# Kernel tuning notes

Hardware: AMD Instinct MI355X
Metric: run time of the kernel (lower is better)

The kernel has to match this reference:

```python
import jax, jax.numpy as jnp
import numpy as np

D_IN, D_HID, D_OUT = 256, 512, 256
N_EXPERTS, TOP_K = 64, 2
B, S = 8, 4096


def setup_inputs() -> dict:
    key = jax.random.key(0)
    ks = jax.random.split(key, 8)
    scale_in = 1.0 / np.sqrt(D_IN)
    scale_hid = 1.0 / np.sqrt(D_HID)
    return {
        "x": jax.random.normal(ks[0], (B, S, D_IN), dtype=jnp.float32),
        "Wr": jax.random.uniform(ks[1], (D_IN, N_EXPERTS), jnp.float32, -scale_in, scale_in),
        "br": jax.random.uniform(ks[2], (N_EXPERTS,), jnp.float32, -scale_in, scale_in),
        "W1": jax.random.uniform(ks[3], (N_EXPERTS, D_IN, D_HID), jnp.float32, -scale_in, scale_in),
        "b1": jax.random.uniform(ks[4], (N_EXPERTS, D_HID), jnp.float32, -scale_in, scale_in),
        "W2": jax.random.uniform(ks[5], (N_EXPERTS, D_HID, D_OUT), jnp.float32, -scale_hid, scale_hid),
        "b2": jax.random.uniform(ks[6], (N_EXPERTS, D_OUT), jnp.float32, -scale_hid, scale_hid),
    }


def reference(x, Wr, br, W1, b1, W2, b2):
    Bx, Sx, D = x.shape
    xf = x.reshape(-1, D)                                  # [T, D]
    T = xf.shape[0]
    E = Wr.shape[1]
    logits = xf @ Wr + br                                  # [T, E]
    topk_logits, topk_idx = jax.lax.top_k(logits, TOP_K)   # [T, K]
    gates = jax.nn.softmax(topk_logits, axis=1)            # softmax over selected k
    # dense combine weights: zero except at selected experts
    combine = jnp.zeros((T, E), xf.dtype).at[
        jnp.arange(T)[:, None], topk_idx].add(gates)       # [T, E]
    out = jnp.zeros((T, W2.shape[-1]), xf.dtype)
    for e in range(E):  # fixed small expert loop; each token weighted by combine mask
        h = jax.nn.relu(xf @ W1[e] + b1[e])                # [T, D_HID]
        y = h @ W2[e] + b2[e]                              # [T, D_OUT]
        out = out + combine[:, e:e + 1] * y
    return out.reshape(Bx, Sx, -1)
```

## Files before the change

### kernel.cpp

```cpp
#include <hip/hip_runtime.h>
#include <stdint.h>

#define T_TOK 32768
#define DIN   256
#define DHID  512
#define DOUT  256
#define NEXP  64
#define L1_SLOTS 8
#define L2_SLOTS 8
#define ROUTER_BLOCKS (T_TOK / 64)
#define PREP_BLOCKS   8192
#define OUTZ_BLOCKS   512
#define XBF_BLOCKS    1024
#define L1_BLOCKS (NEXP * 4 * L1_SLOTS)
#define L2_BLOCKS (NEXP * 2 * L2_SLOTS)

typedef __attribute__((ext_vector_type(8))) short short8;
typedef __attribute__((ext_vector_type(4))) float f32x4;

#define OFF_W1F   0u
#define OFF_W2F   16777216u
#define OFF_BASE  33554432u
#define OFF_CNT   (OFF_BASE + 0u)
#define OFF_CUR   (OFF_BASE + 256u)
#define OFF_OFFS  (OFF_BASE + 512u)
#define OFF_TOPKE (OFF_BASE + 2048u)
#define OFF_TOPKG (OFF_TOPKE + 262144u)
#define OFF_PERM  (OFF_TOPKG + 262144u)
#define OFF_PGATE (OFF_PERM + 262144u)
#define OFF_XBF   (OFF_BASE + 2097152u)
#define OFF_H     (OFF_XBF + 16777216u)

__device__ __forceinline__ unsigned short f2bf(float f) {
    union { float f; unsigned u; } a; a.f = f;
    unsigned u = a.u;
    u += 0x7fffu + ((u >> 16) & 1u);
    return (unsigned short)(u >> 16);
}
__device__ __forceinline__ unsigned pack2(float a, float b) {
    return (unsigned)f2bf(a) | ((unsigned)f2bf(b) << 16);
}

__device__ __forceinline__ void async_copy16(const uint4* g, uint4* l) {
    __builtin_amdgcn_global_load_lds(
        (const __attribute__((address_space(1))) unsigned int*)g,
        (__attribute__((address_space(3))) unsigned int*)l, 16, 0, 0);
}

__global__ __launch_bounds__(256) void router_prep(const float* __restrict__ x,
                                                   const float* __restrict__ Wr,
                                                   const float* __restrict__ br,
                                                   const float* __restrict__ W1,
                                                   const float* __restrict__ W2,
                                                   uint4* __restrict__ W1f,
                                                   uint4* __restrict__ W2f,
                                                   int* __restrict__ topk_e,
                                                   float* __restrict__ topk_g,
                                                   int* __restrict__ cnt,
                                                   float4* __restrict__ outz,
                                                   unsigned* __restrict__ xbf) {
    __shared__ float xl[64][68];
    __shared__ float wt[64][68];
    __shared__ int lcnt[NEXP];
    int tid = threadIdx.x;

    if (blockIdx.x >= ROUTER_BLOCKS + PREP_BLOCKS + OUTZ_BLOCKS) {
        int blk = blockIdx.x - (ROUTER_BLOCKS + PREP_BLOCKS + OUTZ_BLOCKS);
        const float2* xs = (const float2*)x;
#pragma unroll
        for (int k = 0; k < 16; ++k) {
            int o = blk * 4096 + k * 256 + tid;
            float2 v = xs[o];
            xbf[o] = pack2(v.x, v.y);
        }
        return;
    }
    if (blockIdx.x >= ROUTER_BLOCKS + PREP_BLOCKS) {
        int base = (blockIdx.x - (ROUTER_BLOCKS + PREP_BLOCKS)) * 256 + tid;
        float4 z = {0.0f, 0.0f, 0.0f, 0.0f};
#pragma unroll
        for (int i = 0; i < 16; ++i) outz[base + i * (OUTZ_BLOCKS * 256)] = z;
        return;
    }
    if (blockIdx.x >= ROUTER_BLOCKS) {
        int g = (blockIdx.x - ROUTER_BLOCKS) * 256 + tid;
        int isW2 = g >> 20;
        int gg = g & ((1 << 20) - 1);
        int l = gg & 63;
        int t = gg >> 6;
        int e = t >> 8;
        int rem = t & 255;
        int quad = l >> 4, lr = l & 15;
        float v[8];
        if (!isW2) {
            int nt = rem >> 3, kt = rem & 7;
            int kb = kt * 32 + quad * 8;
            int n = nt * 16 + lr;
            const float* s = W1 + (size_t)e * DIN * DHID + n;
#pragma unroll
            for (int j = 0; j < 8; ++j) v[j] = s[(size_t)(kb + j) * DHID];
        } else {
            int nt = rem >> 4, kt = rem & 15;
            int kb = kt * 32 + quad * 8;
            int n = nt * 16 + lr;
            const float* s = W2 + (size_t)e * DHID * DOUT + n;
#pragma unroll
            for (int j = 0; j < 8; ++j) v[j] = s[(size_t)(kb + j) * DOUT];
        }
        uint4 o;
        o.x = pack2(v[0], v[1]); o.y = pack2(v[2], v[3]);
        o.z = pack2(v[4], v[5]); o.w = pack2(v[6], v[7]);
        (isW2 ? W2f : W1f)[gg] = o;
        return;
    }

    if (tid < NEXP) lcnt[tid] = 0;
    int a = tid >> 4;
    int bcol = tid & 15;
    int tok0 = blockIdx.x * 64;
    float c[4][4];
#pragma unroll
    for (int i = 0; i < 4; ++i)
#pragma unroll
        for (int j = 0; j < 4; ++j) c[i][j] = 0.0f;

    for (int chunk = 0; chunk < 4; ++chunk) {
        int d0 = chunk * 64;
        {
            int tok = tid >> 2, off = (tid & 3) * 16;
            const float4* s = (const float4*)(x + (size_t)(tok0 + tok) * DIN + d0 + off);
            float4* d = (float4*)&xl[tok][off];
#pragma unroll
            for (int i = 0; i < 4; ++i) d[i] = s[i];
        }
        {
            int dd = tid >> 2, ecol = (tid & 3) * 16;
            const float* s = Wr + (size_t)(d0 + dd) * NEXP + ecol;
#pragma unroll
            for (int j = 0; j < 16; ++j) wt[ecol + j][dd] = s[j];
        }
        __syncthreads();
#pragma unroll 4
        for (int d = 0; d < 64; d += 4) {
            float4 xv[4], wv[4];
#pragma unroll
            for (int i = 0; i < 4; ++i) xv[i] = *(const float4*)&xl[bcol + i * 16][d];
#pragma unroll
            for (int j = 0; j < 4; ++j) wv[j] = *(const float4*)&wt[a + j * 16][d];
#pragma unroll
            for (int i = 0; i < 4; ++i)
#pragma unroll
                for (int j = 0; j < 4; ++j) {
                    c[i][j] = fmaf(xv[i].x, wv[j].x, c[i][j]);
                    c[i][j] = fmaf(xv[i].y, wv[j].y, c[i][j]);
                    c[i][j] = fmaf(xv[i].z, wv[j].z, c[i][j]);
                    c[i][j] = fmaf(xv[i].w, wv[j].w, c[i][j]);
                }
        }
        __syncthreads();
    }
#pragma unroll
    for (int i = 0; i < 4; ++i)
#pragma unroll
        for (int j = 0; j < 4; ++j)
            xl[bcol + i * 16][a + j * 16] = c[i][j] + br[a + j * 16];
    __syncthreads();

    int w = tid >> 6, lane = tid & 63;
    for (int ti = 0; ti < 16; ++ti) {
        int tl = w * 16 + ti;
        float acc = xl[tl][lane];
        float v = acc; int idx = lane;
#pragma unroll
        for (int m = 32; m; m >>= 1) {
            float ov = __shfl_xor(v, m); int oi = __shfl_xor(idx, m);
            if (ov > v || (ov == v && oi < idx)) { v = ov; idx = oi; }
        }
        int e0 = idx; float l0 = v;
        float v2 = (lane == e0) ? -3.4e38f : acc; int idx2 = lane;
#pragma unroll
        for (int m = 32; m; m >>= 1) {
            float ov = __shfl_xor(v2, m); int oi = __shfl_xor(idx2, m);
            if (ov > v2 || (ov == v2 && oi < idx2)) { v2 = ov; idx2 = oi; }
        }
        if (lane == 0) {
            int t = tok0 + tl;
            float ex = expf(v2 - l0);
            float g1 = ex / (1.0f + ex);
            topk_e[2 * t] = e0; topk_e[2 * t + 1] = idx2;
            topk_g[2 * t] = 1.0f - g1; topk_g[2 * t + 1] = g1;
            atomicAdd(&lcnt[e0], 1);
            atomicAdd(&lcnt[idx2], 1);
        }
    }
    __syncthreads();
    if (tid < NEXP) atomicAdd(&cnt[tid], lcnt[tid]);
}

__global__ __launch_bounds__(256) void scatter_kernel(const int* __restrict__ topk_e,
                                                      const float* __restrict__ topk_g,
                                                      const int* __restrict__ cnt,
                                                      int* __restrict__ cursor,
                                                      int* __restrict__ perm,
                                                      float* __restrict__ pgate,
                                                      int* __restrict__ offs_g) {
    __shared__ int lcnt[NEXP], lbase[NEXP], sOffs[NEXP];
    int tid = threadIdx.x;
    if (tid < NEXP) lcnt[tid] = 0;
    if (tid < 64) {
        int c = cnt[tid];
        int ic = c;
#pragma unroll
        for (int d = 1; d < 64; d <<= 1) {
            int vc = __shfl_up(ic, d);
            if (tid >= d) ic += vc;
        }
        sOffs[tid] = ic - c;
        if (blockIdx.x == 0) {
            offs_g[tid] = ic - c;
            if (tid == 63) offs_g[64] = ic;
        }
    }
    __syncthreads();
    int t = blockIdx.x * 256 + tid;
    int e0 = topk_e[2 * t], e1 = topk_e[2 * t + 1];
    int i0 = atomicAdd(&lcnt[e0], 1);
    int i1 = atomicAdd(&lcnt[e1], 1);
    __syncthreads();
    if (tid < NEXP) lbase[tid] = atomicAdd(&cursor[tid], lcnt[tid]);
    __syncthreads();
    int p0 = sOffs[e0] + lbase[e0] + i0;
    int p1 = sOffs[e1] + lbase[e1] + i1;
    perm[p0] = t; pgate[p0] = topk_g[2 * t];
    perm[p1] = t; pgate[p1] = topk_g[2 * t + 1];
}

__global__ __launch_bounds__(256, 2) void expert_l1(const unsigned short* __restrict__ xbf,
                                                    const uint4* __restrict__ W1f,
                                                    const float* __restrict__ b1,
                                                    const int* __restrict__ cnt,
                                                    const int* __restrict__ offs,
                                                    const int* __restrict__ perm,
                                                    unsigned short* __restrict__ H) {
    __shared__ uint4 Wlds[4096];
    __shared__ int toks[128];
    __shared__ float b1s[128];

    int tid = threadIdx.x, bx = blockIdx.x;
    int ns = bx & 3, slot = (bx >> 2) & 7, e = bx >> 5;
    int ne = cnt[e];
    if (slot * 128 >= ne) return;
    int base = offs[e];
    int w = tid >> 6, lane = tid & 63, quad = lane >> 4, lr = lane & 15;

    const uint4* src = W1f + (size_t)(e * 256 + ns * 64) * 64;
#pragma unroll
    for (int r = 0; r < 16; ++r)
        async_copy16(src + r * 256 + w * 64 + lane, Wlds + r * 256 + w * 64);
    if (tid < 32)
        *(float4*)&b1s[tid * 4] =
            *(const float4*)(b1 + (size_t)e * DHID + ns * 128 + tid * 4);

    for (int mc = slot; mc * 128 < ne; mc += L1_SLOTS) {
        __syncthreads();
        if (tid < 128) {
            int idx = mc * 128 + tid;
            toks[tid] = perm[base + (idx < ne ? idx : ne - 1)];
        }
        __syncthreads();

        short8 a[2][8];
#pragma unroll
        for (int mt = 0; mt < 2; ++mt) {
            const unsigned short* xr =
                xbf + (size_t)toks[(w * 2 + mt) * 16 + lr] * DIN + quad * 8;
#pragma unroll
            for (int kt = 0; kt < 8; ++kt) a[mt][kt] = *(const short8*)(xr + kt * 32);
        }

#pragma unroll
        for (int ntb = 0; ntb < 4; ++ntb) {
            f32x4 acc[2][2];
#pragma unroll
            for (int i = 0; i < 2; ++i)
#pragma unroll
                for (int m = 0; m < 2; ++m) acc[i][m] = (f32x4){0.f, 0.f, 0.f, 0.f};
#pragma unroll
            for (int kt = 0; kt < 8; ++kt) {
                short8 B0 = *(const short8*)&Wlds[((ntb * 2 + 0) * 8 + kt) * 64 + lane];
                short8 B1 = *(const short8*)&Wlds[((ntb * 2 + 1) * 8 + kt) * 64 + lane];
#pragma unroll
                for (int mt = 0; mt < 2; ++mt) {
                    acc[0][mt] = __builtin_amdgcn_mfma_f32_16x16x32_bf16(a[mt][kt], B0, acc[0][mt], 0, 0, 0);
                    acc[1][mt] = __builtin_amdgcn_mfma_f32_16x16x32_bf16(a[mt][kt], B1, acc[1][mt], 0, 0, 0);
                }
            }
#pragma unroll
            for (int nt2 = 0; nt2 < 2; ++nt2) {
                int nloc = ntb * 32 + nt2 * 16 + lr;
                float bias = b1s[nloc];
#pragma unroll
                for (int mt = 0; mt < 2; ++mt)
#pragma unroll
                    for (int r = 0; r < 4; ++r) {
                        int idx = mc * 128 + (w * 2 + mt) * 16 + quad * 4 + r;
                        if (idx < ne)
                            H[(size_t)(base + idx) * DHID + ns * 128 + nloc] =
                                f2bf(fmaxf(acc[nt2][mt][r] + bias, 0.0f));
                    }
            }
        }
    }
}

__global__ __launch_bounds__(256, 2) void expert_l2(const unsigned short* __restrict__ H,
                                                    const uint4* __restrict__ W2f,
                                                    const float* __restrict__ b2,
                                                    const int* __restrict__ cnt,
                                                    const int* __restrict__ offs,
                                                    const int* __restrict__ perm,
                                                    const float* __restrict__ pgate,
                                                    float* __restrict__ out) {
    __shared__ uint4 Wlds[4096];
    __shared__ int toks[128];
    __shared__ float gs[128];
    __shared__ float b2s[128];

    int tid = threadIdx.x, bx = blockIdx.x;
    int ns = bx & 1, slot = (bx >> 1) & 7, e = bx >> 4;
    int ne = cnt[e];
    if (slot * 128 >= ne) return;
    int base = offs[e];
    int w = tid >> 6, lane = tid & 63, quad = lane >> 4, lr = lane & 15;

    if (tid < 32)
        *(float4*)&b2s[tid * 4] =
            *(const float4*)(b2 + (size_t)e * DOUT + ns * 128 + tid * 4);

    for (int mc = slot; mc * 128 < ne; mc += L2_SLOTS) {
        __syncthreads();
        if (tid < 128) {
            int idx = mc * 128 + tid;
            int p = base + (idx < ne ? idx : ne - 1);
            toks[tid] = perm[p];
            gs[tid] = (idx < ne) ? pgate[p] : 0.0f;
        }

        int row0 = mc * 128 + (w * 2 + 0) * 16 + lr;
        int row1 = mc * 128 + (w * 2 + 1) * 16 + lr;
        if (row0 >= ne) row0 = ne - 1;
        if (row1 >= ne) row1 = ne - 1;
        const unsigned short* h0 = H + (size_t)(base + row0) * DHID + quad * 8;
        const unsigned short* h1 = H + (size_t)(base + row1) * DHID + quad * 8;

        f32x4 acc[8][2];
#pragma unroll
        for (int nt = 0; nt < 8; ++nt)
#pragma unroll
            for (int mt = 0; mt < 2; ++mt) acc[nt][mt] = (f32x4){0.f, 0.f, 0.f, 0.f};

#pragma unroll
        for (int kh = 0; kh < 2; ++kh) {
            if (kh) __syncthreads();
#pragma unroll
            for (int nt = 0; nt < 8; ++nt) {
                const uint4* src = W2f + (size_t)(e * 256 + (ns * 8 + nt) * 16 + kh * 8) * 64;
                async_copy16(src + w * 64 + lane, Wlds + nt * 512 + w * 64);
                async_copy16(src + 256 + w * 64 + lane, Wlds + nt * 512 + 256 + w * 64);
            }
            __syncthreads();

            short8 a[8][2];
#pragma unroll
            for (int kt = 0; kt < 8; ++kt) {
                a[kt][0] = *(const short8*)(h0 + kh * 256 + kt * 32);
                a[kt][1] = *(const short8*)(h1 + kh * 256 + kt * 32);
            }
#pragma unroll
            for (int kt = 0; kt < 8; ++kt) {
#pragma unroll
                for (int nt = 0; nt < 8; ++nt) {
                    short8 B = *(const short8*)&Wlds[(nt * 8 + kt) * 64 + lane];
                    acc[nt][0] = __builtin_amdgcn_mfma_f32_16x16x32_bf16(a[kt][0], B, acc[nt][0], 0, 0, 0);
                    acc[nt][1] = __builtin_amdgcn_mfma_f32_16x16x32_bf16(a[kt][1], B, acc[nt][1], 0, 0, 0);
                }
            }
        }

#pragma unroll
        for (int nt = 0; nt < 8; ++nt) {
            int nloc = nt * 16 + lr;
            float bias = b2s[nloc];
#pragma unroll
            for (int mt = 0; mt < 2; ++mt)
#pragma unroll
                for (int r = 0; r < 4; ++r) {
                    int lidx = (w * 2 + mt) * 16 + quad * 4 + r;
                    if (mc * 128 + lidx < ne)
                        atomicAdd(&out[(size_t)toks[lidx] * DOUT + ns * 128 + nloc],
                                  gs[lidx] * (acc[nt][mt][r] + bias));
                }
        }
    }
}

extern "C" void kernel_launch(void* const* d_in, const int* in_sizes, int n_in,
                              void* d_out, int out_size, void* d_ws, size_t ws_size,
                              hipStream_t stream) {
    (void)in_sizes; (void)n_in; (void)ws_size; (void)out_size;
    const float* x  = (const float*)d_in[0];
    const float* Wr = (const float*)d_in[1];
    const float* br = (const float*)d_in[2];
    const float* W1 = (const float*)d_in[3];
    const float* b1 = (const float*)d_in[4];
    const float* W2 = (const float*)d_in[5];
    const float* b2 = (const float*)d_in[6];
    float* out = (float*)d_out;
    char* ws = (char*)d_ws;

    uint4*    W1f    = (uint4*)(ws + OFF_W1F);
    uint4*    W2f    = (uint4*)(ws + OFF_W2F);
    int*      cnt    = (int*)(ws + OFF_CNT);
    int*      cursor = (int*)(ws + OFF_CUR);
    int*      offs   = (int*)(ws + OFF_OFFS);
    int*      topk_e = (int*)(ws + OFF_TOPKE);
    float*    topk_g = (float*)(ws + OFF_TOPKG);
    int*      perm   = (int*)(ws + OFF_PERM);
    float*    pgate  = (float*)(ws + OFF_PGATE);
    unsigned* xbf    = (unsigned*)(ws + OFF_XBF);
    unsigned short* Hbuf = (unsigned short*)(ws + OFF_H);

    hipMemsetAsync(ws + OFF_CNT, 0, 512, stream);

    router_prep<<<ROUTER_BLOCKS + PREP_BLOCKS + OUTZ_BLOCKS + XBF_BLOCKS, 256, 0, stream>>>(
        x, Wr, br, W1, W2, W1f, W2f, topk_e, topk_g, cnt, (float4*)out, xbf);
    scatter_kernel<<<T_TOK / 256, 256, 0, stream>>>(topk_e, topk_g, cnt, cursor,
                                                    perm, pgate, offs);
    expert_l1<<<L1_BLOCKS, 256, 0, stream>>>((const unsigned short*)xbf, W1f, b1,
                                             cnt, offs, perm, Hbuf);
    expert_l2<<<L2_BLOCKS, 256, 0, stream>>>(Hbuf, W2f, b2, cnt, offs, perm, pgate, out);
}
```

Baseline: 306.2 us.

## Replace atomic scatter-add output with bf16 expert outputs and gather combine kernel

```diff
diff --git a/kernel.cpp b/kernel.cpp
--- a/kernel.cpp
+++ b/kernel.cpp
@@ -10,10 +10,10 @@
 #define L2_SLOTS 8
 #define ROUTER_BLOCKS (T_TOK / 64)
 #define PREP_BLOCKS   8192
-#define OUTZ_BLOCKS   512
 #define XBF_BLOCKS    1024
 #define L1_BLOCKS (NEXP * 4 * L1_SLOTS)
 #define L2_BLOCKS (NEXP * 2 * L2_SLOTS)
+#define CMB_BLOCKS (T_TOK / 8)
 
 typedef __attribute__((ext_vector_type(8))) short short8;
 typedef __attribute__((ext_vector_type(4))) float f32x4;
@@ -28,8 +28,10 @@
 #define OFF_TOPKG (OFF_TOPKE + 262144u)
 #define OFF_PERM  (OFF_TOPKG + 262144u)
 #define OFF_PGATE (OFF_PERM + 262144u)
+#define OFF_ISLOT (OFF_PGATE + 262144u)
 #define OFF_XBF   (OFF_BASE + 2097152u)
 #define OFF_H     (OFF_XBF + 16777216u)
+#define OFF_YP    (OFF_H + 67108864u)
 
 __device__ __forceinline__ unsigned short f2bf(float f) {
     union { float f; unsigned u; } a; a.f = f;
@@ -39,6 +41,9 @@
 }
 __device__ __forceinline__ unsigned pack2(float a, float b) {
     return (unsigned)f2bf(a) | ((unsigned)f2bf(b) << 16);
+}
+__device__ __forceinline__ float bf2f(unsigned short u) {
+    union { unsigned u; float f; } a; a.u = (unsigned)u << 16; return a.f;
 }
 
 __device__ __forceinline__ void async_copy16(const uint4* g, uint4* l) {
@@ -57,15 +62,14 @@
                                                    int* __restrict__ topk_e,
                                                    float* __restrict__ topk_g,
                                                    int* __restrict__ cnt,
-                                                   float4* __restrict__ outz,
                                                    unsigned* __restrict__ xbf) {
     __shared__ float xl[64][68];
     __shared__ float wt[64][68];
     __shared__ int lcnt[NEXP];
     int tid = threadIdx.x;
 
-    if (blockIdx.x >= ROUTER_BLOCKS + PREP_BLOCKS + OUTZ_BLOCKS) {
-        int blk = blockIdx.x - (ROUTER_BLOCKS + PREP_BLOCKS + OUTZ_BLOCKS);
+    if (blockIdx.x >= ROUTER_BLOCKS + PREP_BLOCKS) {
+        int blk = blockIdx.x - (ROUTER_BLOCKS + PREP_BLOCKS);
         const float2* xs = (const float2*)x;
 #pragma unroll
         for (int k = 0; k < 16; ++k) {
@@ -73,13 +77,6 @@
             float2 v = xs[o];
             xbf[o] = pack2(v.x, v.y);
         }
-        return;
-    }
-    if (blockIdx.x >= ROUTER_BLOCKS + PREP_BLOCKS) {
-        int base = (blockIdx.x - (ROUTER_BLOCKS + PREP_BLOCKS)) * 256 + tid;
-        float4 z = {0.0f, 0.0f, 0.0f, 0.0f};
-#pragma unroll
-        for (int i = 0; i < 16; ++i) outz[base + i * (OUTZ_BLOCKS * 256)] = z;
         return;
     }
     if (blockIdx.x >= ROUTER_BLOCKS) {
@@ -202,7 +199,7 @@
                                                       const int* __restrict__ cnt,
                                                       int* __restrict__ cursor,
                                                       int* __restrict__ perm,
-                                                      float* __restrict__ pgate,
+                                                      int* __restrict__ islot,
                                                       int* __restrict__ offs_g) {
     __shared__ int lcnt[NEXP], lbase[NEXP], sOffs[NEXP];
     int tid = threadIdx.x;
@@ -231,8 +228,10 @@
     __syncthreads();
     int p0 = sOffs[e0] + lbase[e0] + i0;
     int p1 = sOffs[e1] + lbase[e1] + i1;
-    perm[p0] = t; pgate[p0] = topk_g[2 * t];
-    perm[p1] = t; pgate[p1] = topk_g[2 * t + 1];
+    perm[p0] = t;
+    perm[p1] = t;
+    islot[2 * t] = p0;
+    islot[2 * t + 1] = p1;
 }
 
 __global__ __launch_bounds__(256, 2) void expert_l1(const unsigned short* __restrict__ xbf,
@@ -318,12 +317,8 @@
                                                     const float* __restrict__ b2,
                                                     const int* __restrict__ cnt,
                                                     const int* __restrict__ offs,
-                                                    const int* __restrict__ perm,
-                                                    const float* __restrict__ pgate,
-                                                    float* __restrict__ out) {
+                                                    unsigned short* __restrict__ yp) {
     __shared__ uint4 Wlds[4096];
-    __shared__ int toks[128];
-    __shared__ float gs[128];
     __shared__ float b2s[128];
 
     int tid = threadIdx.x, bx = blockIdx.x;
@@ -338,14 +333,6 @@
             *(const float4*)(b2 + (size_t)e * DOUT + ns * 128 + tid * 4);
 
     for (int mc = slot; mc * 128 < ne; mc += L2_SLOTS) {
-        __syncthreads();
-        if (tid < 128) {
-            int idx = mc * 128 + tid;
-            int p = base + (idx < ne ? idx : ne - 1);
-            toks[tid] = perm[p];
-            gs[tid] = (idx < ne) ? pgate[p] : 0.0f;
-        }
-
         int row0 = mc * 128 + (w * 2 + 0) * 16 + lr;
         int row1 = mc * 128 + (w * 2 + 1) * 16 + lr;
         if (row0 >= ne) row0 = ne - 1;
@@ -361,7 +348,7 @@
 
 #pragma unroll
         for (int kh = 0; kh < 2; ++kh) {
-            if (kh) __syncthreads();
+            __syncthreads();
 #pragma unroll
             for (int nt = 0; nt < 8; ++nt) {
                 const uint4* src = W2f + (size_t)(e * 256 + (ns * 8 + nt) * 16 + kh * 8) * 64;
@@ -395,13 +382,38 @@
             for (int mt = 0; mt < 2; ++mt)
 #pragma unroll
                 for (int r = 0; r < 4; ++r) {
-                    int lidx = (w * 2 + mt) * 16 + quad * 4 + r;
-                    if (mc * 128 + lidx < ne)
-                        atomicAdd(&out[(size_t)toks[lidx] * DOUT + ns * 128 + nloc],
-                                  gs[lidx] * (acc[nt][mt][r] + bias));
+                    int crow = mc * 128 + (w * 2 + mt) * 16 + quad * 4 + r;
+                    if (crow < ne)
+                        yp[(size_t)(base + crow) * DOUT + ns * 128 + nloc] =
+                            f2bf(acc[nt][mt][r] + bias);
                 }
         }
     }
+}
+
+__global__ __launch_bounds__(256) void combine_out(const unsigned short* __restrict__ yp,
+                                                   const int* __restrict__ islot,
+                                                   const float* __restrict__ topk_g,
+                                                   float* __restrict__ out) {
+    int tid = threadIdx.x;
+    int tok = blockIdx.x * 8 + (tid >> 5);
+    int cseg = (tid & 31) * 8;
+    int p0 = islot[2 * tok], p1 = islot[2 * tok + 1];
+    float g0 = topk_g[2 * tok], g1 = topk_g[2 * tok + 1];
+    short8 v0 = *(const short8*)(yp + (size_t)p0 * DOUT + cseg);
+    short8 v1 = *(const short8*)(yp + (size_t)p1 * DOUT + cseg);
+    float4 o0, o1;
+    o0.x = g0 * bf2f((unsigned short)v0[0]) + g1 * bf2f((unsigned short)v1[0]);
+    o0.y = g0 * bf2f((unsigned short)v0[1]) + g1 * bf2f((unsigned short)v1[1]);
+    o0.z = g0 * bf2f((unsigned short)v0[2]) + g1 * bf2f((unsigned short)v1[2]);
+    o0.w = g0 * bf2f((unsigned short)v0[3]) + g1 * bf2f((unsigned short)v1[3]);
+    o1.x = g0 * bf2f((unsigned short)v0[4]) + g1 * bf2f((unsigned short)v1[4]);
+    o1.y = g0 * bf2f((unsigned short)v0[5]) + g1 * bf2f((unsigned short)v1[5]);
+    o1.z = g0 * bf2f((unsigned short)v0[6]) + g1 * bf2f((unsigned short)v1[6]);
+    o1.w = g0 * bf2f((unsigned short)v0[7]) + g1 * bf2f((unsigned short)v1[7]);
+    float* d = out + (size_t)tok * DOUT + cseg;
+    *(float4*)d = o0;
+    *(float4*)(d + 4) = o1;
 }
 
 extern "C" void kernel_launch(void* const* d_in, const int* in_sizes, int n_in,
@@ -426,17 +438,19 @@
     int*      topk_e = (int*)(ws + OFF_TOPKE);
     float*    topk_g = (float*)(ws + OFF_TOPKG);
     int*      perm   = (int*)(ws + OFF_PERM);
-    float*    pgate  = (float*)(ws + OFF_PGATE);
+    int*      islot  = (int*)(ws + OFF_ISLOT);
     unsigned* xbf    = (unsigned*)(ws + OFF_XBF);
     unsigned short* Hbuf = (unsigned short*)(ws + OFF_H);
+    unsigned short* ypb  = (unsigned short*)(ws + OFF_YP);
 
     hipMemsetAsync(ws + OFF_CNT, 0, 512, stream);
 
-    router_prep<<<ROUTER_BLOCKS + PREP_BLOCKS + OUTZ_BLOCKS + XBF_BLOCKS, 256, 0, stream>>>(
-        x, Wr, br, W1, W2, W1f, W2f, topk_e, topk_g, cnt, (float4*)out, xbf);
+    router_prep<<<ROUTER_BLOCKS + PREP_BLOCKS + XBF_BLOCKS, 256, 0, stream>>>(
+        x, Wr, br, W1, W2, W1f, W2f, topk_e, topk_g, cnt, xbf);
     scatter_kernel<<<T_TOK / 256, 256, 0, stream>>>(topk_e, topk_g, cnt, cursor,
-                                                    perm, pgate, offs);
+                                                    perm, islot, offs);
     expert_l1<<<L1_BLOCKS, 256, 0, stream>>>((const unsigned short*)xbf, W1f, b1,
                                              cnt, offs, perm, Hbuf);
-    expert_l2<<<L2_BLOCKS, 256, 0, stream>>>(Hbuf, W2f, b2, cnt, offs, perm, pgate, out);
-}
+    expert_l2<<<L2_BLOCKS, 256, 0, stream>>>(Hbuf, W2f, b2, cnt, offs, ypb);
+    combine_out<<<CMB_BLOCKS, 256, 0, stream>>>(ypb, islot, topk_g, out);
+}
```

Result: faster. 283.3 us (-7.5%).
